# Performance work log

Measured on AMD Instinct MI355X. Metric: run time of the kernel, lower is better.

## Reference

```python
import jax, jax.numpy as jnp
import numpy as np

MAX_N = 32        # mixture degree N
N_PTS = 16384     # number of scalar inputs
INIT_DECAY = 1.0


def setup_inputs() -> dict:
    key = jax.random.key(0)
    k1, _ = jax.random.split(key)
    # inputs assumed elementwise in [-1, 1]
    xs = jax.random.uniform(k1, (N_PTS,), dtype=jnp.float32, minval=-1.0, maxval=1.0)
    # learned logits param, init logits[n] = -n * init_decay (as in __init__)
    logits = -INIT_DECAY * jnp.arange(MAX_N + 1, dtype=jnp.float32)
    return {"xs": xs, "logits": logits}


def _psi(xs, logits, max_n):
    """psi(x) = concat_n sqrt(w_n) * phi_n(x); shape (P, 2*max_n+1).

    phi_0 = [1]; phi_n = [T_n(x), sqrt(1-x^2) * U_{n-1}(x)] for n>=1.
    Single linear-pass recurrence instead of per-degree recompute.
    """
    w = jax.nn.softmax(logits)          # (max_n+1,)
    sw = jnp.sqrt(w)
    xc = jnp.clip(xs, -1.0, 1.0)        # (P,)
    s = jnp.sqrt(jnp.clip(1.0 - xc * xc, 0.0))
    P = xs.shape[0]

    # T_0..T_max_n and U_0..U_max_n via one shared recurrence (fixed small loop)
    Ts = [jnp.ones_like(xc), xc]
    Us = [jnp.ones_like(xc), 2.0 * xc]
    for _ in range(2, max_n + 1):
        Ts.append(2.0 * xc * Ts[-1] - Ts[-2])
        Us.append(2.0 * xc * Us[-1] - Us[-2])
    T = jnp.stack(Ts, axis=-1)          # (P, max_n+1)
    U = jnp.stack(Us, axis=-1)          # (P, max_n+1)

    Tn = T[:, 1:]                       # T_1..T_N            (P, max_n)
    Un = U[:, :max_n]                   # U_0..U_{N-1}        (P, max_n)
    # interleave per degree: [T_n, s * U_{n-1}], weighted by sqrt(w_n)
    pair = jnp.stack([Tn, s[:, None] * Un], axis=-1)   # (P, max_n, 2)
    pair = pair * sw[1:][None, :, None]
    head = sw[0] * jnp.ones((P, 1), dtype=xs.dtype)    # sqrt(w_0) * phi_0
    return jnp.concatenate([head, pair.reshape(P, 2 * max_n)], axis=-1)


def reference(xs, logits):
    """gram(xs) = psi(xs) @ psi(xs)^T, shape (P, P)."""
    psi = _psi(xs, logits, MAX_N)       # (P, 2*MAX_N+1)
    return psi @ psi.T
```

## Files before the change

kernel.cpp:

```cpp
#include <hip/hip_runtime.h>
#include <hip/hip_bf16.h>
#include <math.h>

#define MAXN    32
#define NPTS    16384
#define NPSI    65
#define KPAD    96
#define RSTRIDE 104
#define BT      64
#define ROWB    (RSTRIDE * 2)
#define PANELB  (BT * ROWB)

typedef __attribute__((ext_vector_type(8))) short  bf16x8;
typedef __attribute__((ext_vector_type(4))) float  f32x4;

__device__ inline ushort f2bf(float f) {
    union { float f; unsigned u; } v; v.f = f;
    unsigned u = v.u;
    u += 0x7FFFu + ((u >> 16) & 1u);
    return (ushort)(u >> 16);
}

__global__ __launch_bounds__(256) void psi_kernel(
    const float* __restrict__ xs, const float* __restrict__ logits,
    ushort* __restrict__ psi)
{
    int pt = blockIdx.x * blockDim.x + threadIdx.x;
    if (pt >= NPTS) return;

    float x = xs[pt];
    x = fminf(1.0f, fmaxf(-1.0f, x));
    float s = sqrtf(fmaxf(0.0f, 1.0f - x * x));

    float m = -3.4e38f;
    #pragma unroll
    for (int n = 0; n <= MAXN; ++n) m = fmaxf(m, logits[n]);
    float sum = 0.0f;
    #pragma unroll
    for (int n = 0; n <= MAXN; ++n) sum += __expf(logits[n] - m);
    float inv = 1.0f / sum;

    ushort tmp[RSTRIDE];
    tmp[0] = f2bf(sqrtf(__expf(logits[0] - m) * inv));
    float Tm1 = 1.0f, T = x;
    float Um1 = 1.0f, U = 2.0f * x;
    float tx = 2.0f * x;
    #pragma unroll
    for (int n = 1; n <= MAXN; ++n) {
        float swn = sqrtf(__expf(logits[n] - m) * inv);
        tmp[2 * n - 1] = f2bf(swn * T);
        tmp[2 * n]     = f2bf(swn * (s * Um1));
        float Tn = tx * T - Tm1; Tm1 = T; T = Tn;
        float Un = tx * U - Um1; Um1 = U; U = Un;
    }
    #pragma unroll
    for (int k = NPSI; k < RSTRIDE; ++k) tmp[k] = 0;

    unsigned long long* dst = (unsigned long long*)(psi + (size_t)pt * RSTRIDE);
    const unsigned long long* src = (const unsigned long long*)tmp;
    #pragma unroll
    for (int k = 0; k < RSTRIDE / 4; ++k) dst[k] = src[k];
}

__device__ inline void load_lds16(const void* g, void* l) {
    __builtin_amdgcn_global_load_lds(
        (const __attribute__((address_space(1))) unsigned*)g,
        (__attribute__((address_space(3))) unsigned*)l, 16, 0, 0);
}

__global__ __launch_bounds__(256) void gram_kernel(
    const ushort* __restrict__ psi, float* __restrict__ out)
{
    __shared__ ushort lds[2 * BT * RSTRIDE];

    const int tid  = threadIdx.x;
    const int w    = tid >> 6;
    const int lane = tid & 63;
    const int bi   = blockIdx.y;
    const int bj   = blockIdx.x;

    {
        const char* gA = (const char*)(psi + (size_t)bi * BT * RSTRIDE);
        const char* gB = (const char*)(psi + (size_t)bj * BT * RSTRIDE);
        char* lbase = (char*)lds;
        for (int q = w; q < 26; q += 4) {
            const char* src = (q < 13) ? (gA + q * 1024) : (gB + (q - 13) * 1024);
            load_lds16(src + lane * 16, lbase + q * 1024);
        }
    }
    __syncthreads();

    const int lr = lane & 15;
    const int lk = (lane >> 4) * 8;

    const ushort* aBase = lds + (w * 16 + lr) * RSTRIDE;
    const ushort* bBase = lds + (BT + lr) * RSTRIDE;

    f32x4 acc[4];
    #pragma unroll
    for (int c = 0; c < 4; ++c) acc[c] = (f32x4){0.f, 0.f, 0.f, 0.f};

    #pragma unroll
    for (int ks = 0; ks < 3; ++ks) {
        bf16x8 a = *(const bf16x8*)(aBase + ks * 32 + lk);
        #pragma unroll
        for (int c = 0; c < 4; ++c) {
            bf16x8 b = *(const bf16x8*)(bBase + c * 16 * RSTRIDE + ks * 32 + lk);
            acc[c] = __builtin_amdgcn_mfma_f32_16x16x32_bf16(a, b, acc[c], 0, 0, 0);
        }
    }

    const int r0 = (lane >> 4) * 4;
    #pragma unroll
    for (int r = 0; r < 4; ++r) {
        size_t rowOff = (size_t)(bi * BT + w * 16 + r0 + r) * NPTS + (size_t)bj * BT + lr;
        #pragma unroll
        for (int c = 0; c < 4; ++c) {
            out[rowOff + c * 16] = acc[c][r];
        }
    }
}

extern "C" void kernel_launch(void* const* d_in, const int* in_sizes, int n_in,
                              void* d_out, int out_size, void* d_ws, size_t ws_size,
                              hipStream_t stream) {
    const float* xs     = (const float*)d_in[0];
    const float* logits = (const float*)d_in[1];
    float* out          = (float*)d_out;
    ushort* psi         = (ushort*)d_ws;

    psi_kernel<<<NPTS / 256, 256, 0, stream>>>(xs, logits, psi);

    dim3 grid(NPTS / BT, NPTS / BT);
    gram_kernel<<<grid, 256, 0, stream>>>(psi, out);
}
```

Before: 215.6 us.

## Enlarge gram tile to 128 and store with vectorized nontemporal writes

Doubles the gram output tile from 64x64 to 128x128, so each wave computes a 32x128 slab with 16 accumulators and reuses each B fragment across two A fragments. The MFMA operands are swapped so each lane holds four consecutive output columns, which allows float4 nontemporal stores in place of scalar stores. This targets the store-bound output write of the 1 GiB fp32 result and per-block overhead. The cost is more LDS and registers per block and fewer blocks in the grid.

```diff
diff --git a/kernel.cpp b/kernel.cpp
--- a/kernel.cpp
+++ b/kernel.cpp
@@ -5,11 +5,11 @@
 #define MAXN    32
 #define NPTS    16384
 #define NPSI    65
-#define KPAD    96
 #define RSTRIDE 104
-#define BT      64
+#define BT      128
 #define ROWB    (RSTRIDE * 2)
 #define PANELB  (BT * ROWB)
+#define NCHUNK  (2 * PANELB / 1024)
 
 typedef __attribute__((ext_vector_type(8))) short  bf16x8;
 typedef __attribute__((ext_vector_type(4))) float  f32x4;
@@ -83,8 +83,8 @@
         const char* gA = (const char*)(psi + (size_t)bi * BT * RSTRIDE);
         const char* gB = (const char*)(psi + (size_t)bj * BT * RSTRIDE);
         char* lbase = (char*)lds;
-        for (int q = w; q < 26; q += 4) {
-            const char* src = (q < 13) ? (gA + q * 1024) : (gB + (q - 13) * 1024);
+        for (int q = w; q < NCHUNK; q += 4) {
+            const char* src = (q < 26) ? (gA + q * 1024) : (gB + (q - 26) * 1024);
             load_lds16(src + lane * 16, lbase + q * 1024);
         }
     }
@@ -93,30 +93,35 @@
     const int lr = lane & 15;
     const int lk = (lane >> 4) * 8;
 
-    const ushort* aBase = lds + (w * 16 + lr) * RSTRIDE;
+    const ushort* aBase = lds + (w * 32 + lr) * RSTRIDE;
     const ushort* bBase = lds + (BT + lr) * RSTRIDE;
 
-    f32x4 acc[4];
+    f32x4 acc[2][8];
     #pragma unroll
-    for (int c = 0; c < 4; ++c) acc[c] = (f32x4){0.f, 0.f, 0.f, 0.f};
+    for (int rt = 0; rt < 2; ++rt)
+        #pragma unroll
+        for (int ct = 0; ct < 8; ++ct) acc[rt][ct] = (f32x4){0.f, 0.f, 0.f, 0.f};
 
     #pragma unroll
     for (int ks = 0; ks < 3; ++ks) {
-        bf16x8 a = *(const bf16x8*)(aBase + ks * 32 + lk);
+        bf16x8 a0 = *(const bf16x8*)(aBase + ks * 32 + lk);
+        bf16x8 a1 = *(const bf16x8*)(aBase + 16 * RSTRIDE + ks * 32 + lk);
         #pragma unroll
-        for (int c = 0; c < 4; ++c) {
-            bf16x8 b = *(const bf16x8*)(bBase + c * 16 * RSTRIDE + ks * 32 + lk);
-            acc[c] = __builtin_amdgcn_mfma_f32_16x16x32_bf16(a, b, acc[c], 0, 0, 0);
+        for (int ct = 0; ct < 8; ++ct) {
+            bf16x8 b = *(const bf16x8*)(bBase + ct * 16 * RSTRIDE + ks * 32 + lk);
+            acc[0][ct] = __builtin_amdgcn_mfma_f32_16x16x32_bf16(b, a0, acc[0][ct], 0, 0, 0);
+            acc[1][ct] = __builtin_amdgcn_mfma_f32_16x16x32_bf16(b, a1, acc[1][ct], 0, 0, 0);
         }
     }
 
-    const int r0 = (lane >> 4) * 4;
+    const int cq = (lane >> 4) * 4;
     #pragma unroll
-    for (int r = 0; r < 4; ++r) {
-        size_t rowOff = (size_t)(bi * BT + w * 16 + r0 + r) * NPTS + (size_t)bj * BT + lr;
+    for (int rt = 0; rt < 2; ++rt) {
+        size_t row = (size_t)(bi * BT + w * 32 + rt * 16 + lr);
+        float* rowp = out + row * NPTS + (size_t)bj * BT + cq;
         #pragma unroll
-        for (int c = 0; c < 4; ++c) {
-            out[rowOff + c * 16] = acc[c][r];
+        for (int ct = 0; ct < 8; ++ct) {
+            __builtin_nontemporal_store(acc[rt][ct], (f32x4*)(rowp + ct * 16));
         }
     }
 }
```

Measured after the change: 330.0 us. +53.0%, slower.

## Widen gram tile to 64x128 and stage output through swizzled LDS for vector stores

Applied to the files above, without the earlier changes.

Each block now computes a 64x128 output tile, loading 128 B-panel rows per block and doubling the MFMA accumulators per wave. Results are written to LDS with an XOR swizzle, using transposed MFMA operands so each lane holds four consecutive columns. They are then read back and stored to global memory as fully coalesced float4 row segments instead of scalar strided stores. This targets the write bandwidth of the large fp32 output, at the cost of extra LDS traffic, a barrier, and more registers.

```diff
diff --git a/kernel.cpp b/kernel.cpp
--- a/kernel.cpp
+++ b/kernel.cpp
@@ -5,11 +5,11 @@
 #define MAXN    32
 #define NPTS    16384
 #define NPSI    65
-#define KPAD    96
 #define RSTRIDE 104
-#define BT      64
-#define ROWB    (RSTRIDE * 2)
-#define PANELB  (BT * ROWB)
+#define BTA     64
+#define BTB     128
+#define NROWS   (BTA + BTB)
+#define NCHUNK  (NROWS * RSTRIDE * 2 / 1024)
 
 typedef __attribute__((ext_vector_type(8))) short  bf16x8;
 typedef __attribute__((ext_vector_type(4))) float  f32x4;
@@ -71,7 +71,7 @@
 __global__ __launch_bounds__(256) void gram_kernel(
     const ushort* __restrict__ psi, float* __restrict__ out)
 {
-    __shared__ ushort lds[2 * BT * RSTRIDE];
+    __shared__ ushort lds[NROWS * RSTRIDE];
 
     const int tid  = threadIdx.x;
     const int w    = tid >> 6;
@@ -80,10 +80,10 @@
     const int bj   = blockIdx.x;
 
     {
-        const char* gA = (const char*)(psi + (size_t)bi * BT * RSTRIDE);
-        const char* gB = (const char*)(psi + (size_t)bj * BT * RSTRIDE);
+        const char* gA = (const char*)(psi + (size_t)bi * BTA * RSTRIDE);
+        const char* gB = (const char*)(psi + (size_t)bj * BTB * RSTRIDE);
         char* lbase = (char*)lds;
-        for (int q = w; q < 26; q += 4) {
+        for (int q = w; q < NCHUNK; q += 4) {
             const char* src = (q < 13) ? (gA + q * 1024) : (gB + (q - 13) * 1024);
             load_lds16(src + lane * 16, lbase + q * 1024);
         }
@@ -92,31 +92,48 @@
 
     const int lr = lane & 15;
     const int lk = (lane >> 4) * 8;
+    const int cq = (lane >> 4) * 4;
 
     const ushort* aBase = lds + (w * 16 + lr) * RSTRIDE;
-    const ushort* bBase = lds + (BT + lr) * RSTRIDE;
+    const ushort* bBase = lds + (BTA + lr) * RSTRIDE;
 
-    f32x4 acc[4];
+    f32x4 acc[8];
     #pragma unroll
-    for (int c = 0; c < 4; ++c) acc[c] = (f32x4){0.f, 0.f, 0.f, 0.f};
+    for (int ct = 0; ct < 8; ++ct) acc[ct] = (f32x4){0.f, 0.f, 0.f, 0.f};
 
     #pragma unroll
     for (int ks = 0; ks < 3; ++ks) {
         bf16x8 a = *(const bf16x8*)(aBase + ks * 32 + lk);
         #pragma unroll
-        for (int c = 0; c < 4; ++c) {
-            bf16x8 b = *(const bf16x8*)(bBase + c * 16 * RSTRIDE + ks * 32 + lk);
-            acc[c] = __builtin_amdgcn_mfma_f32_16x16x32_bf16(a, b, acc[c], 0, 0, 0);
+        for (int ct = 0; ct < 8; ++ct) {
+            bf16x8 b = *(const bf16x8*)(bBase + ct * 16 * RSTRIDE + ks * 32 + lk);
+            acc[ct] = __builtin_amdgcn_mfma_f32_16x16x32_bf16(b, a, acc[ct], 0, 0, 0);
         }
     }
 
-    const int r0 = (lane >> 4) * 4;
-    #pragma unroll
-    for (int r = 0; r < 4; ++r) {
-        size_t rowOff = (size_t)(bi * BT + w * 16 + r0 + r) * NPTS + (size_t)bj * BT + lr;
+    __syncthreads();
+    float* ldsF = (float*)lds;
+    {
+        const int row = w * 16 + lr;
+        const int rx  = (row & 7) << 2;
         #pragma unroll
-        for (int c = 0; c < 4; ++c) {
-            out[rowOff + c * 16] = acc[c][r];
+        for (int ct = 0; ct < 8; ++ct) {
+            int col = (cq + ct * 16) ^ rx;
+            *(f32x4*)(ldsF + row * BTB + col) = acc[ct];
+        }
+    }
+    __syncthreads();
+
+    {
+        const int rsub = tid >> 5;
+        const int col  = (tid & 31) * 4;
+        #pragma unroll
+        for (int p = 0; p < 8; ++p) {
+            int row  = p * 8 + rsub;
+            int colr = col ^ ((row & 7) << 2);
+            f32x4 v = *(const f32x4*)(ldsF + row * BTB + colr);
+            float* dst = out + (size_t)(bi * BTA + row) * NPTS + (size_t)bj * BTB + col;
+            *(f32x4*)dst = v;
         }
     }
 }
@@ -131,6 +148,6 @@
 
     psi_kernel<<<NPTS / 256, 256, 0, stream>>>(xs, logits, psi);
 
-    dim3 grid(NPTS / BT, NPTS / BT);
+    dim3 grid(NPTS / BTB, NPTS / BTA);
     gram_kernel<<<grid, 256, 0, stream>>>(psi, out);
 }
```

After: 190.7 us. 1.13x faster.
